# Optimization experiments

Measured on AMD Instinct MI355X. Metric: run time of the kernel, lower is better.

The kernel has to match this reference:

```python
import jax, jax.numpy as jnp
import numpy as np

B, T, D = 8, 1024, 256
H, KD = 8, 256          # keras MHA built with key_dim=embed_dim -> per-head dim = D
FF = 1024
WIN = 64                # causal sliding window size
G = 2                   # num_global_tokens (last-k tokens of the sequence)
EPS = 1e-6
NEG = -1e9


def _mha(q_in, kv_in, Wq, bq, Wk, bk, Wv, bv, Wo, bo, mask=None):
    """Keras-style MultiHeadAttention. q_in:[B,Tq,D], kv_in:[B,Ts,D] -> [B,Tq,D]."""
    q = jnp.einsum('btd,dhk->bthk', q_in, Wq) + bq
    k = jnp.einsum('bsd,dhk->bshk', kv_in, Wk) + bk
    v = jnp.einsum('bsd,dhk->bshk', kv_in, Wv) + bv
    s = jnp.einsum('bthk,bshk->bhts', q, k) / jnp.sqrt(jnp.asarray(KD, q.dtype))
    if mask is not None:
        s = jnp.where(mask, s, jnp.asarray(NEG, s.dtype))
    a = jax.nn.softmax(s, axis=-1)
    o = jnp.einsum('bhts,bshk->bthk', a, v)
    return jnp.einsum('bthk,hkd->btd', o, Wo) + bo


def _ln(x, g, b):
    m = jnp.mean(x, axis=-1, keepdims=True)
    v = jnp.mean(jnp.square(x - m), axis=-1, keepdims=True)
    return (x - m) * jax.lax.rsqrt(v + EPS) * g + b


def setup_inputs() -> dict:
    key = jax.random.key(0)
    ks = jax.random.split(key, 32)
    sp = 1.0 / np.sqrt(D)   # proj fan-in D
    so = 1.0 / np.sqrt(H * KD)

    def mha_params(k0):
        k = jax.random.split(k0, 4)
        return dict(
            Wq=jax.random.normal(k[0], (D, H, KD), jnp.float32) * sp,
            Wk=jax.random.normal(k[1], (D, H, KD), jnp.float32) * sp,
            Wv=jax.random.normal(k[2], (D, H, KD), jnp.float32) * sp,
            Wo=jax.random.normal(k[3], (H, KD, D), jnp.float32) * so,
        )
    lp = mha_params(ks[1])
    gp = mha_params(ks[2])
    inp = {
        'x': jax.random.normal(ks[0], (B, T, D), jnp.float32),
        'lWq': lp['Wq'], 'lbq': jnp.zeros((H, KD), jnp.float32),
        'lWk': lp['Wk'], 'lbk': jnp.zeros((H, KD), jnp.float32),
        'lWv': lp['Wv'], 'lbv': jnp.zeros((H, KD), jnp.float32),
        'lWo': lp['Wo'], 'lbo': jnp.zeros((D,), jnp.float32),
        'gWq': gp['Wq'], 'gbq': jnp.zeros((H, KD), jnp.float32),
        'gWk': gp['Wk'], 'gbk': jnp.zeros((H, KD), jnp.float32),
        'gWv': gp['Wv'], 'gbv': jnp.zeros((H, KD), jnp.float32),
        'gWo': gp['Wo'], 'gbo': jnp.zeros((D,), jnp.float32),
        'fW1': jax.random.normal(ks[3], (D, FF), jnp.float32) * sp,
        'fb1': jnp.zeros((FF,), jnp.float32),
        'fW2': jax.random.normal(ks[4], (FF, D), jnp.float32) * (1.0 / np.sqrt(FF)),
        'fb2': jnp.zeros((D,), jnp.float32),
        'ln1_g': jnp.ones((D,), jnp.float32), 'ln1_b': jnp.zeros((D,), jnp.float32),
        'ln2_g': jnp.ones((D,), jnp.float32), 'ln2_b': jnp.zeros((D,), jnp.float32),
    }
    return inp


def reference(x, lWq, lbq, lWk, lbk, lWv, lbv, lWo, lbo,
              gWq, gbq, gWk, gbk, gWv, gbv, gWo, gbo,
              fW1, fb1, fW2, fb2, ln1_g, ln1_b, ln2_g, ln2_b):
    i = jnp.arange(T)[:, None]
    j = jnp.arange(T)[None, :]
    win_mask = (j <= i) & (j > i - WIN)            # [T,T]
    win_mask = win_mask[None, None]                # [1,1,T,T]

    # Local window attention (the original per-timestep loop, fused via mask).
    local = _mha(x, x, lWq, lbq, lWk, lbk, lWv, lbv, lWo, lbo, mask=win_mask)

    # Global tokens: last G tokens attend to full sequence, then tokens attend to them.
    g = x[:, T - G:, :]                            # [B,G,D]
    g2 = _mha(g, x, gWq, gbq, gWk, gbk, gWv, gbv, gWo, gbo)
    gx = _mha(x, g2, gWq, gbq, gWk, gbk, gWv, gbv, gWo, gbo)

    attn_out = local + gx
    out1 = _ln(x + attn_out, ln1_g, ln1_b)
    ffn = jnp.maximum(out1 @ fW1 + fb1, 0.0) @ fW2 + fb2
    return _ln(out1 + ffn, ln2_g, ln2_b)
```

## Files before the change

kernel.cpp:

```cpp
#include <hip/hip_runtime.h>
#include <hip/hip_bf16.h>

#define B_ 8
#define T_ 1024
#define D_ 256
#define H_ 8
#define KD_ 256
#define HK_ 2048
#define FF_ 1024
#define WIN_ 64
#define BT_ 8192
#define S6_ 6144
#define S4_ 4096

using bf16 = __hip_bfloat16;
typedef float f32x4 __attribute__((ext_vector_type(4)));
typedef short s16x8 __attribute__((ext_vector_type(8)));

__device__ inline float b2f(bf16 h) { return __bfloat162float(h); }
__device__ inline float bs2f(short s) {
    unsigned int u = ((unsigned int)(unsigned short)s) << 16;
    return __builtin_bit_cast(float, u);
}
__device__ inline float us2f(unsigned short s) {
    unsigned int u = ((unsigned int)s) << 16;
    return __builtin_bit_cast(float, u);
}
__device__ inline unsigned short fbits(float x) { bf16 h = __float2bfloat16(x); return __builtin_bit_cast(unsigned short, h); }

__device__ __forceinline__ void stage16(const void* g, void* l) {
    __builtin_amdgcn_global_load_lds((const __attribute__((address_space(1))) void*)g,
                                     (__attribute__((address_space(3))) void*)l, 16, 0, 0);
}

__global__ __launch_bounds__(256) void f32_to_bf16_vec(const float* __restrict__ in, bf16* __restrict__ out, int n) {
    int i = (blockIdx.x * 256 + threadIdx.x) * 4;
    if (i + 3 < n) {
        float4 v = *(const float4*)(in + i);
        ushort4 o;
        o.x = fbits(v.x); o.y = fbits(v.y); o.z = fbits(v.z); o.w = fbits(v.w);
        *(ushort4*)(out + i) = o;
    }
}

struct TJob { const float* in; bf16* out; int R; int C; int os; int tile_start; };
struct TJobs { TJob j[10]; int total; };

__global__ void transpose_all(TJobs js) {
    __shared__ float tile[32][33];
    int bid = blockIdx.x;
    int ji = 0;
    while (ji < 9 && bid >= js.j[ji + 1].tile_start) ji++;
    TJob jb = js.j[ji];
    int t = bid - jb.tile_start;
    int tiles_x = jb.C / 32;
    int cb = (t % tiles_x) * 32, rb = (t / tiles_x) * 32;
    for (int k = 0; k < 4; k++) {
        int r = threadIdx.y + k * 8;
        tile[r][threadIdx.x] = jb.in[(size_t)(rb + r) * jb.C + cb + threadIdx.x];
    }
    __syncthreads();
    for (int k = 0; k < 4; k++) {
        int r = threadIdx.y + k * 8;
        jb.out[(size_t)(cb + r) * jb.os + rb + threadIdx.x] = __float2bfloat16(tile[threadIdx.x][r]);
    }
}

__global__ __launch_bounds__(256) void concat_bias(const float* a0, const float* a1, const float* a2,
                                                   const float* b0, const float* b1,
                                                   float* outL, float* outG) {
    int i = blockIdx.x * 256 + threadIdx.x;
    int seg = i >> 11, off = i & 2047;
    outL[i] = (seg == 0 ? a0 : seg == 1 ? a1 : a2)[off];
    if (i < 4096) outG[i] = (seg == 0 ? b0 : b1)[off];
}

template <int MODE, int BN>
__global__ __launch_bounds__(256) void gemm128(const bf16* __restrict__ A, const bf16* __restrict__ Bt,
                                               const float* __restrict__ bias, bf16* __restrict__ C,
                                               int M, int N, int K) {
    constexpr int NF = BN / 32;
    constexpr int ABUF = 128 * 64;
    constexpr int BBUF = BN * 64;
    constexpr int BUFE = ABUF + BBUF;
    constexpr int EC = BN + 8;
    constexpr int ARENA_E = (2 * BUFE > 128 * EC) ? 2 * BUFE : 128 * EC;
    __shared__ __align__(16) bf16 arena[ARENA_E];
    const int tid = threadIdx.x;
    const int w = tid >> 6, l = tid & 63;
    const int m0 = blockIdx.y * 128, n0 = blockIdx.x * BN;
    const int wm = (w >> 1) * 64, wn = (w & 1) * (BN / 2);
    const int srow = w * 8 + (l >> 3);
    const int scol = ((l & 7) ^ (l >> 3)) * 8;
    const int ldsOff = w * 512;
    const int nt = K / 64;

    auto stageT = [&](int buf, int k0) {
        bf16* Ad = arena + buf * BUFE;
        bf16* Bd = Ad + ABUF;
#pragma unroll
        for (int j = 0; j < 4; j++)
            stage16(A + (size_t)(m0 + j * 32 + srow) * K + k0 + scol, &Ad[ldsOff + j * 2048]);
#pragma unroll
        for (int j = 0; j < NF; j++)
            stage16(Bt + (size_t)(n0 + j * 32 + srow) * K + k0 + scol, &Bd[ldsOff + j * 2048]);
    };

    f32x4 acc[4][NF] = {};
    stageT(0, 0);
    __syncthreads();
    int cur = 0;
    for (int t = 0; t < nt; t++) {
        if (t + 1 < nt) stageT(cur ^ 1, (t + 1) * 64);
        const bf16* As = arena + cur * BUFE;
        const bf16* Bs = As + ABUF;
#pragma unroll
        for (int ks = 0; ks < 2; ks++) {
            s16x8 a[4], b[NF];
#pragma unroll
            for (int mf = 0; mf < 4; mf++) {
                int ar = wm + mf * 16 + (l & 15);
                int ch = (ks * 4 + (l >> 4)) ^ (ar & 7);
                a[mf] = *(const s16x8*)&As[ar * 64 + ch * 8];
            }
#pragma unroll
            for (int nf = 0; nf < NF; nf++) {
                int br = wn + nf * 16 + (l & 15);
                int ch = (ks * 4 + (l >> 4)) ^ (br & 7);
                b[nf] = *(const s16x8*)&Bs[br * 64 + ch * 8];
            }
            __builtin_amdgcn_s_setprio(1);
#pragma unroll
            for (int mf = 0; mf < 4; mf++)
#pragma unroll
                for (int nf = 0; nf < NF; nf++)
                    acc[mf][nf] = __builtin_amdgcn_mfma_f32_16x16x32_bf16(a[mf], b[nf], acc[mf][nf], 0, 0, 0);
            __builtin_amdgcn_s_setprio(0);
        }
        __syncthreads();
        cur ^= 1;
    }
    bf16* Es = arena;
#pragma unroll
    for (int mf = 0; mf < 4; mf++)
#pragma unroll
        for (int nf = 0; nf < NF; nf++)
#pragma unroll
            for (int r = 0; r < 4; r++) {
                int row = wm + mf * 16 + (l >> 4) * 4 + r;
                int col = wn + nf * 16 + (l & 15);
                float v = acc[mf][nf][r] + bias[n0 + col];
                if (MODE == 2) v = fmaxf(v, 0.f);
                Es[row * EC + col] = __float2bfloat16(v);
            }
    __syncthreads();
    constexpr int RPC = BN / 8;
    constexpr int CPT = (128 * BN) / (256 * 8);
#pragma unroll
    for (int c = 0; c < CPT; c++) {
        int lin = c * 256 + tid;
        int row = lin / RPC, cc = lin - row * RPC;
        s16x8 v = *(const s16x8*)&Es[row * EC + cc * 8];
        *(s16x8*)(C + (size_t)(m0 + row) * N + n0 + cc * 8) = v;
    }
}

__global__ __launch_bounds__(256) void local_attn(const bf16* __restrict__ QKV, bf16* __restrict__ O) {
    __shared__ bf16 U[256 * 72];
    __shared__ bf16 Ps[64][136];
    const int tid = threadIdx.x, l = tid & 63, w = tid >> 6;
    const int qt = blockIdx.x, bh = blockIdx.y;
    const int b = bh >> 3, h = bh & 7;
    const int qs = qt * 64;
    const int r0 = w * 16;
    const int lrow = tid >> 2, lc4 = (tid & 3) * 8;
    const size_t obase = (size_t)b * T_ * HK_ + h * KD_;

    s16x8 qa[8];
    {
        const bf16* qbase = QKV + (size_t)(b * T_ + qs + r0 + (l & 15)) * S6_ + h * KD_ + (l >> 4) * 8;
#pragma unroll
        for (int ks = 0; ks < 8; ks++) qa[ks] = *(const s16x8*)(qbase + ks * 32);
    }

    bf16(*Ks)[264] = (bf16(*)[264])U;
    {
        int tk = qs - 64 + lrow;
        const bf16* krow = QKV + (size_t)(b * T_ + tk) * S6_ + 2048 + h * KD_;
#pragma unroll
        for (int c = 0; c < 8; c++) {
            int col = lc4 + c * 32;
            uint4 val = {0, 0, 0, 0};
            if (tk >= 0) val = *(const uint4*)(krow + col);
            *(uint4*)&Ks[lrow][col] = val;
        }
    }
    __syncthreads();
    f32x4 sacc[8];
#pragma unroll
    for (int f = 0; f < 8; f++) sacc[f] = (f32x4){0.f, 0.f, 0.f, 0.f};
    __builtin_amdgcn_s_setprio(1);
#pragma unroll
    for (int nf = 0; nf < 4; nf++)
#pragma unroll
        for (int ks = 0; ks < 8; ks++) {
            s16x8 bb = *(const s16x8*)&Ks[nf * 16 + (l & 15)][ks * 32 + (l >> 4) * 8];
            sacc[nf] = __builtin_amdgcn_mfma_f32_16x16x32_bf16(qa[ks], bb, sacc[nf], 0, 0, 0);
        }
    __builtin_amdgcn_s_setprio(0);
    __syncthreads();
    {
        const bf16* krow = QKV + (size_t)(b * T_ + qs + lrow) * S6_ + 2048 + h * KD_;
#pragma unroll
        for (int c = 0; c < 8; c++) {
            int col = lc4 + c * 32;
            *(uint4*)&Ks[lrow][col] = *(const uint4*)(krow + col);
        }
    }
    __syncthreads();
    __builtin_amdgcn_s_setprio(1);
#pragma unroll
    for (int nf = 0; nf < 4; nf++)
#pragma unroll
        for (int ks = 0; ks < 8; ks++) {
            s16x8 bb = *(const s16x8*)&Ks[nf * 16 + (l & 15)][ks * 32 + (l >> 4) * 8];
            sacc[4 + nf] = __builtin_amdgcn_mfma_f32_16x16x32_bf16(qa[ks], bb, sacc[4 + nf], 0, 0, 0);
        }
    __builtin_amdgcn_s_setprio(0);

    uint4 vreg[8];
    {
        int tk = qs - 64 + lrow;
        const bf16* vrow = QKV + (size_t)(b * T_ + tk) * S6_ + 4096 + h * KD_;
#pragma unroll
        for (int c = 0; c < 8; c++) {
            uint4 v = {0, 0, 0, 0};
            if (tk >= 0) v = *(const uint4*)(vrow + lc4 + c * 32);
            vreg[c] = v;
        }
    }

#pragma unroll
    for (int r = 0; r < 4; r++) {
        int i = qs + r0 + (l >> 4) * 4 + r;
#pragma unroll
        for (int f = 0; f < 8; f++) {
            int j = qs - 64 + f * 16 + (l & 15);
            bool valid = (j >= 0) && (j <= i) && (j > i - WIN_);
            sacc[f][r] = valid ? sacc[f][r] * (1.f / 16.f) : -1e9f;
        }
        float mm = -1e30f;
#pragma unroll
        for (int f = 0; f < 8; f++) mm = fmaxf(mm, sacc[f][r]);
        mm = fmaxf(mm, __shfl_xor(mm, 1, 64));
        mm = fmaxf(mm, __shfl_xor(mm, 2, 64));
        mm = fmaxf(mm, __shfl_xor(mm, 4, 64));
        mm = fmaxf(mm, __shfl_xor(mm, 8, 64));
        float ss = 0.f;
#pragma unroll
        for (int f = 0; f < 8; f++) {
            float e = __expf(sacc[f][r] - mm);
            sacc[f][r] = e;
            ss += e;
        }
        ss += __shfl_xor(ss, 1, 64);
        ss += __shfl_xor(ss, 2, 64);
        ss += __shfl_xor(ss, 4, 64);
        ss += __shfl_xor(ss, 8, 64);
        float inv = 1.f / ss;
#pragma unroll
        for (int f = 0; f < 8; f++) sacc[f][r] *= inv;
    }
    __syncthreads();

    bf16(*VT)[72] = (bf16(*)[72])U;
#pragma unroll
    for (int f = 0; f < 8; f++)
#pragma unroll
        for (int r = 0; r < 4; r++)
            Ps[r0 + (l >> 4) * 4 + r][f * 16 + (l & 15)] = __float2bfloat16(sacc[f][r]);
#pragma unroll
    for (int c = 0; c < 8; c++) {
        int col = lc4 + c * 32;
        bf16 tmp[8];
        *(uint4*)tmp = vreg[c];
        for (int e = 0; e < 8; e++) VT[col + e][lrow] = tmp[e];
    }
    __syncthreads();
    {
        const bf16* vrow = QKV + (size_t)(b * T_ + qs + lrow) * S6_ + 4096 + h * KD_;
#pragma unroll
        for (int c = 0; c < 8; c++) vreg[c] = *(const uint4*)(vrow + lc4 + c * 32);
    }

    f32x4 oacc[16];
#pragma unroll
    for (int nf = 0; nf < 16; nf++) oacc[nf] = (f32x4){0.f, 0.f, 0.f, 0.f};
    for (int kb = 0; kb < 2; kb++) {
#pragma unroll
        for (int ks = 0; ks < 2; ks++) {
            s16x8 a = *(const s16x8*)&Ps[r0 + (l & 15)][kb * 64 + ks * 32 + (l >> 4) * 8];
            __builtin_amdgcn_s_setprio(1);
#pragma unroll
            for (int nf = 0; nf < 16; nf++) {
                s16x8 bb = *(const s16x8*)&VT[nf * 16 + (l & 15)][ks * 32 + (l >> 4) * 8];
                oacc[nf] = __builtin_amdgcn_mfma_f32_16x16x32_bf16(a, bb, oacc[nf], 0, 0, 0);
            }
            __builtin_amdgcn_s_setprio(0);
        }
        if (kb == 0) {
            __syncthreads();
#pragma unroll
            for (int c = 0; c < 8; c++) {
                int col = lc4 + c * 32;
                bf16 tmp[8];
                *(uint4*)tmp = vreg[c];
                for (int e = 0; e < 8; e++) VT[col + e][lrow] = tmp[e];
            }
            __syncthreads();
        }
    }
#pragma unroll
    for (int nf = 0; nf < 16; nf++)
#pragma unroll
        for (int r = 0; r < 4; r++) {
            int row = r0 + (l >> 4) * 4 + r;
            int col = nf * 16 + (l & 15);
            O[obase + (size_t)(qs + row) * HK_ + col] = __float2bfloat16(oacc[nf][r]);
        }
}

__global__ __launch_bounds__(256) void qg_kernel(const float* __restrict__ x, const bf16* __restrict__ gwq_t,
                                                 const float* __restrict__ gbq, float* __restrict__ qg) {
    __shared__ float xs[256];
    int bi = blockIdx.x, ch = blockIdx.y, tid = threadIdx.x;
    int b = bi >> 1, i = bi & 1;
    xs[tid] = x[((size_t)b * T_ + (T_ - 2 + i)) * D_ + tid];
    __syncthreads();
    int hk = ch * 256 + tid;
    const bf16* wr = gwq_t + (size_t)hk * D_;
    float acc = gbq[hk];
    for (int c = 0; c < 32; c++) {
        s16x8 wv = *(const s16x8*)&wr[c * 8];
#pragma unroll
        for (int e = 0; e < 8; e++) acc += xs[c * 8 + e] * bs2f(wv[e]);
    }
    qg[(size_t)bi * HK_ + hk] = acc;
}

__global__ __launch_bounds__(256) void g2_scores(const float* __restrict__ qg, const bf16* __restrict__ KVg,
                                                 float* __restrict__ sc) {
    __shared__ float qf[2][256];
    int bh = blockIdx.x, ch = blockIdx.y;
    int b = bh >> 3, h = bh & 7;
    int tid = threadIdx.x;
    for (int i = 0; i < 2; i++)
        qf[i][tid] = qg[(size_t)(b * 2 + i) * HK_ + h * KD_ + tid];
    __syncthreads();
    int t = ch * 256 + tid;
    const bf16* kr = &KVg[((size_t)(b * T_ + t)) * S4_ + h * KD_];
    float a0 = 0.f, a1 = 0.f;
    for (int c = 0; c < 32; c++) {
        s16x8 kv = *(const s16x8*)&kr[c * 8];
#pragma unroll
        for (int e = 0; e < 8; e++) {
            float kf = bs2f(kv[e]);
            a0 += kf * qf[0][c * 8 + e];
            a1 += kf * qf[1][c * 8 + e];
        }
    }
    sc[((size_t)bh * 2 + 0) * T_ + t] = a0 * (1.f / 16.f);
    sc[((size_t)bh * 2 + 1) * T_ + t] = a1 * (1.f / 16.f);
}

__global__ __launch_bounds__(256) void g2_softmax(float* __restrict__ sc) {
    __shared__ float red[4];
    int bh = blockIdx.x, tid = threadIdx.x;
    int w = tid >> 6;
    for (int i = 0; i < 2; i++) {
        float* row = &sc[((size_t)bh * 2 + i) * T_];
        float vals[4];
        float m = -1e30f;
        for (int c = 0; c < 4; c++) {
            vals[c] = row[tid + 256 * c];
            m = fmaxf(m, vals[c]);
        }
        for (int s = 32; s >= 1; s >>= 1) m = fmaxf(m, __shfl_xor(m, s, 64));
        if ((tid & 63) == 0) red[w] = m;
        __syncthreads();
        m = fmaxf(fmaxf(red[0], red[1]), fmaxf(red[2], red[3]));
        __syncthreads();
        float s = 0.f;
        for (int c = 0; c < 4; c++) {
            vals[c] = __expf(vals[c] - m);
            s += vals[c];
        }
        for (int d = 32; d >= 1; d >>= 1) s += __shfl_xor(s, d, 64);
        if ((tid & 63) == 0) red[w] = s;
        __syncthreads();
        s = red[0] + red[1] + red[2] + red[3];
        float inv = 1.f / s;
        for (int c = 0; c < 4; c++) row[tid + 256 * c] = vals[c] * inv;
        __syncthreads();
    }
}

__global__ __launch_bounds__(256) void g2_pv(const float* __restrict__ sc, const bf16* __restrict__ KVg,
                                             float* __restrict__ og_part) {
    __shared__ float p2[2][256];
    int bh = blockIdx.x, ch = blockIdx.y;
    int b = bh >> 3, h = bh & 7;
    int tid = threadIdx.x;
    for (int i = 0; i < 2; i++) p2[i][tid] = sc[((size_t)bh * 2 + i) * T_ + ch * 256 + tid];
    __syncthreads();
    const bf16* vb = &KVg[((size_t)(b * T_ + ch * 256)) * S4_ + 2048 + h * KD_ + tid];
    float a0 = 0.f, a1 = 0.f;
    for (int t = 0; t < 256; t++) {
        float vv = b2f(vb[(size_t)t * S4_]);
        a0 += p2[0][t] * vv;
        a1 += p2[1][t] * vv;
    }
    og_part[((size_t)(bh * 4 + ch) * 2 + 0) * KD_ + tid] = a0;
    og_part[((size_t)(bh * 4 + ch) * 2 + 1) * KD_ + tid] = a1;
}

__global__ __launch_bounds__(256) void g2_red(const float* __restrict__ og_part, float* __restrict__ og2) {
    int idx = blockIdx.x * 256 + threadIdx.x;
    int kd = idx & 255, i = (idx >> 8) & 1, h = (idx >> 9) & 7, b = idx >> 12;
    int bh = b * 8 + h;
    float s = 0.f;
    for (int ch = 0; ch < 4; ch++) s += og_part[((size_t)(bh * 4 + ch) * 2 + i) * KD_ + kd];
    og2[(size_t)(b * 2 + i) * 2048 + h * 256 + kd] = s;
}

__global__ __launch_bounds__(256) void g2_lin(const float* __restrict__ og2, const bf16* __restrict__ gwoT,
                                              const float* __restrict__ gbo, float* __restrict__ g2buf) {
    int bi = blockIdx.x, tid = threadIdx.x;
    int d = blockIdx.y * 16 + (tid >> 4);
    int s16i = tid & 15;
    const float* ogr = og2 + (size_t)bi * 2048 + s16i * 128;
    const bf16* wr = gwoT + (size_t)d * HK_ + s16i * 128;
    float acc = 0.f;
    for (int c = 0; c < 16; c++) {
        s16x8 wv = *(const s16x8*)&wr[c * 8];
#pragma unroll
        for (int e = 0; e < 8; e++) acc += ogr[c * 8 + e] * bs2f(wv[e]);
    }
    acc += __shfl_xor(acc, 1, 64);
    acc += __shfl_xor(acc, 2, 64);
    acc += __shfl_xor(acc, 4, 64);
    acc += __shfl_xor(acc, 8, 64);
    if (s16i == 0) g2buf[(size_t)bi * 256 + d] = acc + gbo[d];
}

__global__ __launch_bounds__(256) void g2_kv(const float* __restrict__ g2buf, const bf16* __restrict__ gwk_t,
                                             const float* __restrict__ gbk, const bf16* __restrict__ gwv_t,
                                             const float* __restrict__ gbv, bf16* __restrict__ K2,
                                             bf16* __restrict__ V2) {
    __shared__ float g2s[256];
    int bi = blockIdx.x, ch = blockIdx.y;
    int tid = threadIdx.x;
    g2s[tid] = g2buf[(size_t)bi * 256 + tid];
    __syncthreads();
    int hk = ch * 256 + tid;
    const bf16* rk = &gwk_t[(size_t)hk * D_];
    const bf16* rv = &gwv_t[(size_t)hk * D_];
    float ak = gbk[hk], av = gbv[hk];
    for (int c = 0; c < 32; c++) {
        s16x8 kw = *(const s16x8*)&rk[c * 8];
        s16x8 vw = *(const s16x8*)&rv[c * 8];
#pragma unroll
        for (int e = 0; e < 8; e++) {
            float g = g2s[c * 8 + e];
            ak += g * bs2f(kw[e]);
            av += g * bs2f(vw[e]);
        }
    }
    K2[(size_t)bi * HK_ + hk] = __float2bfloat16(ak);
    V2[(size_t)bi * HK_ + hk] = __float2bfloat16(av);
}

__global__ __launch_bounds__(256) void a2w2_kernel(const bf16* __restrict__ K2, const bf16* __restrict__ V2,
                                                   const bf16* __restrict__ gwq_t, const bf16* __restrict__ gwoT,
                                                   const float* __restrict__ gbq, float* __restrict__ A2,
                                                   float* __restrict__ W2, float* __restrict__ c2) {
    __shared__ float k2s[256], v2s[256];
    __shared__ float red[4];
    int bi = blockIdx.x, h = blockIdx.y, tid = threadIdx.x;
    k2s[tid] = b2f(K2[(size_t)bi * HK_ + h * 256 + tid]);
    v2s[tid] = b2f(V2[(size_t)bi * HK_ + h * 256 + tid]);
    __syncthreads();
    float accA = 0.f;
    const bf16* wq = gwq_t + (size_t)(h * 256) * D_ + tid;
    for (int kd = 0; kd < 256; kd++)
        accA += k2s[kd] * b2f(wq[(size_t)kd * D_]);
    float accW = 0.f;
    const bf16* wo = gwoT + (size_t)tid * HK_ + h * 256;
    for (int c = 0; c < 32; c++) {
        s16x8 wv = *(const s16x8*)&wo[c * 8];
#pragma unroll
        for (int e = 0; e < 8; e++) accW += v2s[c * 8 + e] * bs2f(wv[e]);
    }
    int o = (bi * 8 + h) * 256 + tid;
    A2[o] = accA;
    W2[o] = accW;
    float pc = gbq[h * 256 + tid] * k2s[tid];
#pragma unroll
    for (int m = 32; m >= 1; m >>= 1) pc += __shfl_xor(pc, m, 64);
    if ((tid & 63) == 0) red[tid >> 6] = pc;
    __syncthreads();
    if (tid == 0) c2[bi * 8 + h] = red[0] + red[1] + red[2] + red[3];
}

__global__ __launch_bounds__(256) void gx_fused(const float* __restrict__ x, const float* __restrict__ A2,
                                                const float* __restrict__ W2, const float* __restrict__ c2,
                                                const float* __restrict__ gbo, bf16* __restrict__ attnG) {
    int w = threadIdx.x >> 6, l = threadIdx.x & 63;
    int t = blockIdx.x * 4 + w;
    int b = t >> 10;
    float4 x4 = *(const float4*)(x + (size_t)t * D_ + l * 4);
    float p[8][2];
#pragma unroll
    for (int h = 0; h < 8; h++)
#pragma unroll
        for (int i = 0; i < 2; i++) {
            const float* a = A2 + ((size_t)((b * 2 + i) * 8 + h)) * 256 + l * 4;
            float4 a4 = *(const float4*)a;
            float dt = x4.x * a4.x + x4.y * a4.y + x4.z * a4.z + x4.w * a4.w;
#pragma unroll
            for (int m = 32; m >= 1; m >>= 1) dt += __shfl_xor(dt, m, 64);
            p[h][i] = dt;
        }
    float4 gb = *(const float4*)(gbo + l * 4);
    float o0 = gb.x, o1 = gb.y, o2 = gb.z, o3 = gb.w;
#pragma unroll
    for (int h = 0; h < 8; h++) {
        float s0 = (p[h][0] + c2[(b * 2 + 0) * 8 + h]) * (1.f / 16.f);
        float s1 = (p[h][1] + c2[(b * 2 + 1) * 8 + h]) * (1.f / 16.f);
        float mx = fmaxf(s0, s1);
        float e0 = __expf(s0 - mx), e1 = __expf(s1 - mx);
        float inv = 1.f / (e0 + e1);
        float p0 = e0 * inv, p1 = e1 * inv;
        float4 w0 = *(const float4*)(W2 + ((size_t)((b * 2 + 0) * 8 + h)) * 256 + l * 4);
        float4 w1 = *(const float4*)(W2 + ((size_t)((b * 2 + 1) * 8 + h)) * 256 + l * 4);
        o0 += p0 * w0.x + p1 * w1.x;
        o1 += p0 * w0.y + p1 * w1.y;
        o2 += p0 * w0.z + p1 * w1.z;
        o3 += p0 * w0.w + p1 * w1.w;
    }
    ushort4 ou;
    ou.x = fbits(o0); ou.y = fbits(o1); ou.z = fbits(o2); ou.w = fbits(o3);
    *(ushort4*)(attnG + (size_t)t * D_ + l * 4) = ou;
}

template <typename TA, bool HASC>
__global__ __launch_bounds__(256) void ln_kernel(const TA* __restrict__ a, const bf16* __restrict__ b2,
                                                 const bf16* __restrict__ c, const float* __restrict__ g,
                                                 const float* __restrict__ bia, float* __restrict__ outf,
                                                 bf16* __restrict__ outb) {
    int w = threadIdx.x >> 6, l = threadIdx.x & 63;
    int row = blockIdx.x * 4 + w;
    size_t base = (size_t)row * D_ + l * 4;
    float vv[4];
    if constexpr (sizeof(TA) == 4) {
        float4 av = *(const float4*)((const float*)a + base);
        vv[0] = av.x; vv[1] = av.y; vv[2] = av.z; vv[3] = av.w;
    } else {
        ushort4 av = *(const ushort4*)((const unsigned short*)a + base);
        vv[0] = us2f(av.x); vv[1] = us2f(av.y); vv[2] = us2f(av.z); vv[3] = us2f(av.w);
    }
    ushort4 bv = *(const ushort4*)((const unsigned short*)b2 + base);
    vv[0] += us2f(bv.x); vv[1] += us2f(bv.y); vv[2] += us2f(bv.z); vv[3] += us2f(bv.w);
    if constexpr (HASC) {
        ushort4 cv = *(const ushort4*)((const unsigned short*)c + base);
        vv[0] += us2f(cv.x); vv[1] += us2f(cv.y); vv[2] += us2f(cv.z); vv[3] += us2f(cv.w);
    }
    float s = vv[0] + vv[1] + vv[2] + vv[3];
#pragma unroll
    for (int m = 32; m >= 1; m >>= 1) s += __shfl_xor(s, m, 64);
    float mean = s * (1.f / 256.f);
    float q = 0.f;
#pragma unroll
    for (int e = 0; e < 4; e++) {
        float d = vv[e] - mean;
        q += d * d;
    }
#pragma unroll
    for (int m = 32; m >= 1; m >>= 1) q += __shfl_xor(q, m, 64);
    float rs = rsqrtf(q * (1.f / 256.f) + 1e-6f);
    float4 gv = *(const float4*)(g + l * 4);
    float4 biv = *(const float4*)(bia + l * 4);
    float o0 = (vv[0] - mean) * rs * gv.x + biv.x;
    float o1 = (vv[1] - mean) * rs * gv.y + biv.y;
    float o2 = (vv[2] - mean) * rs * gv.z + biv.z;
    float o3 = (vv[3] - mean) * rs * gv.w + biv.w;
    if (outf) *(float4*)(outf + base) = (float4){o0, o1, o2, o3};
    if (outb) {
        ushort4 ou;
        ou.x = fbits(o0); ou.y = fbits(o1); ou.z = fbits(o2); ou.w = fbits(o3);
        *(ushort4*)(outb + base) = ou;
    }
}

extern "C" void kernel_launch(void* const* d_in, const int* in_sizes, int n_in, void* d_out, int out_size,
                              void* d_ws, size_t ws_size, hipStream_t stream) {
    const float* x = (const float*)d_in[0];
    const float* lWq = (const float*)d_in[1];  const float* lbq = (const float*)d_in[2];
    const float* lWk = (const float*)d_in[3];  const float* lbk = (const float*)d_in[4];
    const float* lWv = (const float*)d_in[5];  const float* lbv = (const float*)d_in[6];
    const float* lWo = (const float*)d_in[7];  const float* lbo = (const float*)d_in[8];
    const float* gWq = (const float*)d_in[9];  const float* gbq = (const float*)d_in[10];
    const float* gWk = (const float*)d_in[11]; const float* gbk = (const float*)d_in[12];
    const float* gWv = (const float*)d_in[13]; const float* gbv = (const float*)d_in[14];
    const float* gWo = (const float*)d_in[15]; const float* gbo = (const float*)d_in[16];
    const float* fW1 = (const float*)d_in[17]; const float* fb1 = (const float*)d_in[18];
    const float* fW2 = (const float*)d_in[19]; const float* fb2 = (const float*)d_in[20];
    const float* ln1g = (const float*)d_in[21]; const float* ln1b = (const float*)d_in[22];
    const float* ln2g = (const float*)d_in[23]; const float* ln2b = (const float*)d_in[24];

    char* ws = (char*)d_ws;
    size_t off = 0;
    auto alloc = [&](size_t bytes) -> char* {
        char* p = ws + off;
        off = (off + bytes + 255) & ~(size_t)255;
        return p;
    };
    bf16* xb = (bf16*)alloc((size_t)BT_ * D_ * 2);
    bf16* WcatL = (bf16*)alloc((size_t)S6_ * D_ * 2);
    bf16* WcatG = (bf16*)alloc((size_t)S4_ * D_ * 2);
    bf16* gwq_t = (bf16*)alloc((size_t)HK_ * D_ * 2);
    bf16* woL = (bf16*)alloc((size_t)D_ * HK_ * 2);
    bf16* gwoT = (bf16*)alloc((size_t)D_ * HK_ * 2);
    bf16* fw1_t = (bf16*)alloc((size_t)FF_ * D_ * 2);
    bf16* fw2_t = (bf16*)alloc((size_t)D_ * FF_ * 2);
    float* bcatL = (float*)alloc((size_t)S6_ * 4);
    float* bcatG = (float*)alloc((size_t)S4_ * 4);
    bf16* QKV = (bf16*)alloc((size_t)BT_ * S6_ * 2);
    bf16* Ob = (bf16*)alloc((size_t)BT_ * HK_ * 2);
    bf16* attnL = (bf16*)alloc((size_t)BT_ * D_ * 2);
    bf16* attnG = (bf16*)alloc((size_t)BT_ * D_ * 2);
    float* sc = (float*)alloc((size_t)B_ * H_ * 2 * T_ * 4);
    float* og_part = (float*)alloc((size_t)B_ * H_ * 4 * 2 * KD_ * 4);
    float* og2 = (float*)alloc((size_t)B_ * 2 * HK_ * 4);
    float* g2buf = (float*)alloc((size_t)B_ * 2 * D_ * 4);
    float* qg = (float*)alloc((size_t)B_ * 2 * HK_ * 4);
    bf16* K2 = (bf16*)alloc((size_t)B_ * 2 * HK_ * 2);
    bf16* V2 = (bf16*)alloc((size_t)B_ * 2 * HK_ * 2);
    float* A2 = (float*)alloc((size_t)16 * 8 * 256 * 4);
    float* W2 = (float*)alloc((size_t)16 * 8 * 256 * 4);
    float* c2 = (float*)alloc((size_t)16 * 8 * 4);
    bf16* KVg = QKV;
    bf16* hid = QKV;
    bf16* ffn = (bf16*)((char*)QKV + (32u << 20));
    bf16* out1b = (bf16*)((char*)QKV + (48u << 20));

    f32_to_bf16_vec<<<(BT_ * D_) / 1024, 256, 0, stream>>>(x, xb, BT_ * D_);
    {
        TJobs js;
        int t = 0;
        auto add = [&](int i, const float* in, bf16* out, int R, int C, int os) {
            js.j[i] = {in, out, R, C, os, t};
            t += (R / 32) * (C / 32);
        };
        add(0, lWq, WcatL, D_, HK_, D_);
        add(1, lWk, WcatL + (size_t)2048 * D_, D_, HK_, D_);
        add(2, lWv, WcatL + (size_t)4096 * D_, D_, HK_, D_);
        add(3, gWk, WcatG, D_, HK_, D_);
        add(4, gWv, WcatG + (size_t)2048 * D_, D_, HK_, D_);
        add(5, gWq, gwq_t, D_, HK_, D_);
        add(6, lWo, woL, HK_, D_, HK_);
        add(7, gWo, gwoT, HK_, D_, HK_);
        add(8, fW1, fw1_t, D_, FF_, D_);
        add(9, fW2, fw2_t, FF_, D_, FF_);
        js.total = t;
        transpose_all<<<t, dim3(32, 8), 0, stream>>>(js);
    }
    concat_bias<<<S6_ / 256, 256, 0, stream>>>(lbq, lbk, lbv, gbk, gbv, bcatL, bcatG);
    qg_kernel<<<dim3(16, 8), 256, 0, stream>>>(x, gwq_t, gbq, qg);

    gemm128<1, 128><<<dim3(S6_ / 128, BT_ / 128), 256, 0, stream>>>(xb, WcatL, bcatL, QKV, BT_, S6_, D_);
    local_attn<<<dim3(T_ / 64, B_ * H_), 256, 0, stream>>>(QKV, Ob);
    gemm128<1, 64><<<dim3(D_ / 64, BT_ / 128), 256, 0, stream>>>(Ob, woL, lbo, attnL, BT_, D_, HK_);

    gemm128<1, 128><<<dim3(S4_ / 128, BT_ / 128), 256, 0, stream>>>(xb, WcatG, bcatG, KVg, BT_, S4_, D_);
    g2_scores<<<dim3(B_ * H_, T_ / 256), 256, 0, stream>>>(qg, KVg, sc);
    g2_softmax<<<B_ * H_, 256, 0, stream>>>(sc);
    g2_pv<<<dim3(B_ * H_, 4), 256, 0, stream>>>(sc, KVg, og_part);
    g2_red<<<128, 256, 0, stream>>>(og_part, og2);
    g2_lin<<<dim3(B_ * 2, 16), 256, 0, stream>>>(og2, gwoT, gbo, g2buf);
    g2_kv<<<dim3(B_ * 2, HK_ / 256), 256, 0, stream>>>(g2buf, WcatG, gbk, WcatG + (size_t)2048 * D_, gbv, K2, V2);
    a2w2_kernel<<<dim3(16, 8), 256, 0, stream>>>(K2, V2, gwq_t, gwoT, gbq, A2, W2, c2);
    gx_fused<<<BT_ / 4, 256, 0, stream>>>(x, A2, W2, c2, gbo, attnG);

    ln_kernel<float, true><<<BT_ / 4, 256, 0, stream>>>(x, attnL, attnG, ln1g, ln1b, nullptr, out1b);
    gemm128<2, 128><<<dim3(FF_ / 128, BT_ / 128), 256, 0, stream>>>(out1b, fw1_t, fb1, hid, BT_, FF_, D_);
    gemm128<1, 64><<<dim3(D_ / 64, BT_ / 128), 256, 0, stream>>>(hid, fw2_t, fb2, ffn, BT_, D_, FF_);
    ln_kernel<bf16, false><<<BT_ / 4, 256, 0, stream>>>(out1b, ffn, nullptr, ln2g, ln2b, (float*)d_out, nullptr);
}
```

Before: 271.6 us.

## Halve GEMM K-tile, use narrower N tiles, fuse global attention kernels

The shared GEMM now stages 32-wide K slices with a new swizzle, and the output-projection and FFN2 GEMMs switch to 32-column tiles, which doubles their block count for better occupancy at small N. The four global-token attention kernels (scores, softmax, PV, reduction) are merged into one kernel per batch-head that keeps scores in shared memory. This removes three launches and the intermediate global buffers. The cost is that the fused kernel runs only 64 blocks with a serial 1024-step PV loop, and the smaller K tile means more barriers per GEMM.

```diff
diff --git a/kernel.cpp b/kernel.cpp
--- a/kernel.cpp
+++ b/kernel.cpp
@@ -80,30 +80,40 @@
                                                const float* __restrict__ bias, bf16* __restrict__ C,
                                                int M, int N, int K) {
     constexpr int NF = BN / 32;
-    constexpr int ABUF = 128 * 64;
-    constexpr int BBUF = BN * 64;
+    constexpr int ABUF = 128 * 32;
+    constexpr int BBUF = BN * 32;
     constexpr int BUFE = ABUF + BBUF;
     constexpr int EC = BN + 8;
     constexpr int ARENA_E = (2 * BUFE > 128 * EC) ? 2 * BUFE : 128 * EC;
+    constexpr int BCH = BN * 4;
     __shared__ __align__(16) bf16 arena[ARENA_E];
     const int tid = threadIdx.x;
     const int w = tid >> 6, l = tid & 63;
     const int m0 = blockIdx.y * 128, n0 = blockIdx.x * BN;
     const int wm = (w >> 1) * 64, wn = (w & 1) * (BN / 2);
-    const int srow = w * 8 + (l >> 3);
-    const int scol = ((l & 7) ^ (l >> 3)) * 8;
-    const int ldsOff = w * 512;
-    const int nt = K / 64;
+    const int nt = K / 32;
 
     auto stageT = [&](int buf, int k0) {
         bf16* Ad = arena + buf * BUFE;
         bf16* Bd = Ad + ABUF;
 #pragma unroll
-        for (int j = 0; j < 4; j++)
-            stage16(A + (size_t)(m0 + j * 32 + srow) * K + k0 + scol, &Ad[ldsOff + j * 2048]);
-#pragma unroll
-        for (int j = 0; j < NF; j++)
-            stage16(Bt + (size_t)(n0 + j * 32 + srow) * K + k0 + scol, &Bd[ldsOff + j * 2048]);
+        for (int j = 0; j < 2; j++) {
+            int cbase = j * 256 + w * 64;
+            int chunk = cbase + l;
+            int row = chunk >> 2, cc = chunk & 3;
+            int sc_ = (cc ^ ((row >> 1) & 3)) * 8;
+            stage16(A + (size_t)(m0 + row) * K + k0 + sc_, Ad + (size_t)cbase * 8);
+        }
+#pragma unroll
+        for (int j = 0; j < (BCH + 255) / 256; j++) {
+            int cbase = j * 256 + w * 64;
+            if (BCH % 256 == 0 || cbase < BCH) {
+                int chunk = cbase + l;
+                int row = chunk >> 2, cc = chunk & 3;
+                int sc_ = (cc ^ ((row >> 1) & 3)) * 8;
+                stage16(Bt + (size_t)(n0 + row) * K + k0 + sc_, Bd + (size_t)cbase * 8);
+            }
+        }
     };
 
     f32x4 acc[4][NF] = {};
@@ -111,32 +121,29 @@
     __syncthreads();
     int cur = 0;
     for (int t = 0; t < nt; t++) {
-        if (t + 1 < nt) stageT(cur ^ 1, (t + 1) * 64);
+        if (t + 1 < nt) stageT(cur ^ 1, (t + 1) * 32);
         const bf16* As = arena + cur * BUFE;
         const bf16* Bs = As + ABUF;
-#pragma unroll
-        for (int ks = 0; ks < 2; ks++) {
-            s16x8 a[4], b[NF];
-#pragma unroll
-            for (int mf = 0; mf < 4; mf++) {
-                int ar = wm + mf * 16 + (l & 15);
-                int ch = (ks * 4 + (l >> 4)) ^ (ar & 7);
-                a[mf] = *(const s16x8*)&As[ar * 64 + ch * 8];
-            }
-#pragma unroll
-            for (int nf = 0; nf < NF; nf++) {
-                int br = wn + nf * 16 + (l & 15);
-                int ch = (ks * 4 + (l >> 4)) ^ (br & 7);
-                b[nf] = *(const s16x8*)&Bs[br * 64 + ch * 8];
-            }
-            __builtin_amdgcn_s_setprio(1);
-#pragma unroll
-            for (int mf = 0; mf < 4; mf++)
-#pragma unroll
-                for (int nf = 0; nf < NF; nf++)
-                    acc[mf][nf] = __builtin_amdgcn_mfma_f32_16x16x32_bf16(a[mf], b[nf], acc[mf][nf], 0, 0, 0);
-            __builtin_amdgcn_s_setprio(0);
-        }
+        s16x8 a[4], b[NF];
+#pragma unroll
+        for (int mf = 0; mf < 4; mf++) {
+            int ar = wm + mf * 16 + (l & 15);
+            int ch = (l >> 4) ^ ((ar >> 1) & 3);
+            a[mf] = *(const s16x8*)&As[ar * 32 + ch * 8];
+        }
+#pragma unroll
+        for (int nf = 0; nf < NF; nf++) {
+            int br = wn + nf * 16 + (l & 15);
+            int ch = (l >> 4) ^ ((br >> 1) & 3);
+            b[nf] = *(const s16x8*)&Bs[br * 32 + ch * 8];
+        }
+        __builtin_amdgcn_s_setprio(1);
+#pragma unroll
+        for (int mf = 0; mf < 4; mf++)
+#pragma unroll
+            for (int nf = 0; nf < NF; nf++)
+                acc[mf][nf] = __builtin_amdgcn_mfma_f32_16x16x32_bf16(a[mf], b[nf], acc[mf][nf], 0, 0, 0);
+        __builtin_amdgcn_s_setprio(0);
         __syncthreads();
         cur ^= 1;
     }
@@ -348,41 +355,39 @@
     qg[(size_t)bi * HK_ + hk] = acc;
 }
 
-__global__ __launch_bounds__(256) void g2_scores(const float* __restrict__ qg, const bf16* __restrict__ KVg,
-                                                 float* __restrict__ sc) {
+__global__ __launch_bounds__(256) void g2_attn(const float* __restrict__ qg, const bf16* __restrict__ KVg,
+                                               float* __restrict__ og2) {
     __shared__ float qf[2][256];
-    int bh = blockIdx.x, ch = blockIdx.y;
+    __shared__ float sc[2][1024];
+    __shared__ float red[4];
+    int bh = blockIdx.x, tid = threadIdx.x;
     int b = bh >> 3, h = bh & 7;
-    int tid = threadIdx.x;
+    int w = tid >> 6;
     for (int i = 0; i < 2; i++)
         qf[i][tid] = qg[(size_t)(b * 2 + i) * HK_ + h * KD_ + tid];
     __syncthreads();
-    int t = ch * 256 + tid;
-    const bf16* kr = &KVg[((size_t)(b * T_ + t)) * S4_ + h * KD_];
-    float a0 = 0.f, a1 = 0.f;
-    for (int c = 0; c < 32; c++) {
-        s16x8 kv = *(const s16x8*)&kr[c * 8];
-#pragma unroll
-        for (int e = 0; e < 8; e++) {
-            float kf = bs2f(kv[e]);
-            a0 += kf * qf[0][c * 8 + e];
-            a1 += kf * qf[1][c * 8 + e];
-        }
-    }
-    sc[((size_t)bh * 2 + 0) * T_ + t] = a0 * (1.f / 16.f);
-    sc[((size_t)bh * 2 + 1) * T_ + t] = a1 * (1.f / 16.f);
-}
-
-__global__ __launch_bounds__(256) void g2_softmax(float* __restrict__ sc) {
-    __shared__ float red[4];
-    int bh = blockIdx.x, tid = threadIdx.x;
-    int w = tid >> 6;
+    for (int chn = 0; chn < 4; chn++) {
+        int t = chn * 256 + tid;
+        const bf16* kr = &KVg[((size_t)(b * T_ + t)) * S4_ + h * KD_];
+        float a0 = 0.f, a1 = 0.f;
+        for (int c = 0; c < 32; c++) {
+            s16x8 kv = *(const s16x8*)&kr[c * 8];
+#pragma unroll
+            for (int e = 0; e < 8; e++) {
+                float kf = bs2f(kv[e]);
+                a0 += kf * qf[0][c * 8 + e];
+                a1 += kf * qf[1][c * 8 + e];
+            }
+        }
+        sc[0][t] = a0 * (1.f / 16.f);
+        sc[1][t] = a1 * (1.f / 16.f);
+    }
+    __syncthreads();
     for (int i = 0; i < 2; i++) {
-        float* row = &sc[((size_t)bh * 2 + i) * T_];
         float vals[4];
         float m = -1e30f;
         for (int c = 0; c < 4; c++) {
-            vals[c] = row[tid + 256 * c];
+            vals[c] = sc[i][tid + 256 * c];
             m = fmaxf(m, vals[c]);
         }
         for (int s = 32; s >= 1; s >>= 1) m = fmaxf(m, __shfl_xor(m, s, 64));
@@ -400,37 +405,18 @@
         __syncthreads();
         s = red[0] + red[1] + red[2] + red[3];
         float inv = 1.f / s;
-        for (int c = 0; c < 4; c++) row[tid + 256 * c] = vals[c] * inv;
+        for (int c = 0; c < 4; c++) sc[i][tid + 256 * c] = vals[c] * inv;
         __syncthreads();
     }
-}
-
-__global__ __launch_bounds__(256) void g2_pv(const float* __restrict__ sc, const bf16* __restrict__ KVg,
-                                             float* __restrict__ og_part) {
-    __shared__ float p2[2][256];
-    int bh = blockIdx.x, ch = blockIdx.y;
-    int b = bh >> 3, h = bh & 7;
-    int tid = threadIdx.x;
-    for (int i = 0; i < 2; i++) p2[i][tid] = sc[((size_t)bh * 2 + i) * T_ + ch * 256 + tid];
-    __syncthreads();
-    const bf16* vb = &KVg[((size_t)(b * T_ + ch * 256)) * S4_ + 2048 + h * KD_ + tid];
     float a0 = 0.f, a1 = 0.f;
-    for (int t = 0; t < 256; t++) {
+    const bf16* vb = &KVg[((size_t)(b * T_)) * S4_ + 2048 + h * KD_ + tid];
+    for (int t = 0; t < 1024; t++) {
         float vv = b2f(vb[(size_t)t * S4_]);
-        a0 += p2[0][t] * vv;
-        a1 += p2[1][t] * vv;
-    }
-    og_part[((size_t)(bh * 4 + ch) * 2 + 0) * KD_ + tid] = a0;
-    og_part[((size_t)(bh * 4 + ch) * 2 + 1) * KD_ + tid] = a1;
-}
-
-__global__ __launch_bounds__(256) void g2_red(const float* __restrict__ og_part, float* __restrict__ og2) {
-    int idx = blockIdx.x * 256 + threadIdx.x;
-    int kd = idx & 255, i = (idx >> 8) & 1, h = (idx >> 9) & 7, b = idx >> 12;
-    int bh = b * 8 + h;
-    float s = 0.f;
-    for (int ch = 0; ch < 4; ch++) s += og_part[((size_t)(bh * 4 + ch) * 2 + i) * KD_ + kd];
-    og2[(size_t)(b * 2 + i) * 2048 + h * 256 + kd] = s;
+        a0 += sc[0][t] * vv;
+        a1 += sc[1][t] * vv;
+    }
+    og2[(size_t)(b * 2 + 0) * 2048 + h * 256 + tid] = a0;
+    og2[(size_t)(b * 2 + 1) * 2048 + h * 256 + tid] = a1;
 }
 
 __global__ __launch_bounds__(256) void g2_lin(const float* __restrict__ og2, const bf16* __restrict__ gwoT,
@@ -639,8 +625,6 @@
     bf16* Ob = (bf16*)alloc((size_t)BT_ * HK_ * 2);
     bf16* attnL = (bf16*)alloc((size_t)BT_ * D_ * 2);
     bf16* attnG = (bf16*)alloc((size_t)BT_ * D_ * 2);
-    float* sc = (float*)alloc((size_t)B_ * H_ * 2 * T_ * 4);
-    float* og_part = (float*)alloc((size_t)B_ * H_ * 4 * 2 * KD_ * 4);
     float* og2 = (float*)alloc((size_t)B_ * 2 * HK_ * 4);
     float* g2buf = (float*)alloc((size_t)B_ * 2 * D_ * 4);
     float* qg = (float*)alloc((size_t)B_ * 2 * HK_ * 4);
@@ -680,13 +664,10 @@
 
     gemm128<1, 128><<<dim3(S6_ / 128, BT_ / 128), 256, 0, stream>>>(xb, WcatL, bcatL, QKV, BT_, S6_, D_);
     local_attn<<<dim3(T_ / 64, B_ * H_), 256, 0, stream>>>(QKV, Ob);
-    gemm128<1, 64><<<dim3(D_ / 64, BT_ / 128), 256, 0, stream>>>(Ob, woL, lbo, attnL, BT_, D_, HK_);
+    gemm128<1, 32><<<dim3(D_ / 32, BT_ / 128), 256, 0, stream>>>(Ob, woL, lbo, attnL, BT_, D_, HK_);
 
     gemm128<1, 128><<<dim3(S4_ / 128, BT_ / 128), 256, 0, stream>>>(xb, WcatG, bcatG, KVg, BT_, S4_, D_);
-    g2_scores<<<dim3(B_ * H_, T_ / 256), 256, 0, stream>>>(qg, KVg, sc);
-    g2_softmax<<<B_ * H_, 256, 0, stream>>>(sc);
-    g2_pv<<<dim3(B_ * H_, 4), 256, 0, stream>>>(sc, KVg, og_part);
-    g2_red<<<128, 256, 0, stream>>>(og_part, og2);
+    g2_attn<<<B_ * H_, 256, 0, stream>>>(qg, KVg, og2);
     g2_lin<<<dim3(B_ * 2, 16), 256, 0, stream>>>(og2, gwoT, gbo, g2buf);
     g2_kv<<<dim3(B_ * 2, HK_ / 256), 256, 0, stream>>>(g2buf, WcatG, gbk, WcatG + (size_t)2048 * D_, gbv, K2, V2);
     a2w2_kernel<<<dim3(16, 8), 256, 0, stream>>>(K2, V2, gwq_t, gwoT, gbq, A2, W2, c2);
@@ -694,6 +675,6 @@
 
     ln_kernel<float, true><<<BT_ / 4, 256, 0, stream>>>(x, attnL, attnG, ln1g, ln1b, nullptr, out1b);
     gemm128<2, 128><<<dim3(FF_ / 128, BT_ / 128), 256, 0, stream>>>(out1b, fw1_t, fb1, hid, BT_, FF_, D_);
-    gemm128<1, 64><<<dim3(D_ / 64, BT_ / 128), 256, 0, stream>>>(hid, fw2_t, fb2, ffn, BT_, D_, FF_);
+    gemm128<1, 32><<<dim3(D_ / 32, BT_ / 128), 256, 0, stream>>>(hid, fw2_t, fb2, ffn, BT_, D_, FF_);
     ln_kernel<bf16, false><<<BT_ / 4, 256, 0, stream>>>(out1b, ffn, nullptr, ln2g, ln2b, (float*)d_out, nullptr);
 }
```

New measurement: 332.2 us. +22.3%, slower.
